# Optimization experiments

Measured on AMD Instinct MI355X. Metric: run time of the kernel, lower is better.

## Reference

```python
import jax, jax.numpy as jnp
import numpy as np

B, S, H, MAX_LEN = 32, 1024, 384, 8192


def setup_inputs() -> dict:
    key = jax.random.key(0)
    k0, k1, k2 = jax.random.split(key, 3)
    x = jax.random.normal(k0, (B, S, H), dtype=jnp.float32)
    src_mask = jnp.ones((B, S), dtype=bool)
    mel_mask = jnp.ones((B, MAX_LEN), dtype=bool)
    duration_target = jax.random.randint(k1, (B, S), 0, 8)
    pitch_target = jax.random.normal(k2, (B, MAX_LEN), dtype=jnp.float32)
    return {
        "x": x,
        "src_mask": src_mask,
        "mel_mask": mel_mask,
        "duration_target": duration_target,
        "pitch_target": pitch_target,
        "max_len": MAX_LEN,
    }


def _length_regulate(x, duration, max_len):
    """Vectorized repeat_interleave + pad.

    Frame t of batch b copies source vector j where
    cumsum(duration)[b, j-1] <= t < cumsum(duration)[b, j].
    """
    cum = jnp.cumsum(duration, axis=1)                      # [B, S]
    mel_len = cum[:, -1]                                    # [B]
    t = jnp.arange(max_len)                                 # [MAX]
    # searchsorted(side='right') maps frame index -> source index
    idx = jax.vmap(lambda c: jnp.searchsorted(c, t, side="right"))(cum)  # [B, MAX]
    idx = jnp.minimum(idx, x.shape[1] - 1)
    out = jnp.take_along_axis(x, idx[:, :, None], axis=1)   # [B, MAX, H]
    valid = t[None, :] < mel_len[:, None]                   # [B, MAX]  (zero padding)
    out = jnp.where(valid[:, :, None], out, jnp.zeros((), out.dtype))
    return out, mel_len


def reference(x, src_mask, mel_mask, duration_target, pitch_target, max_len):
    out, mel_len = _length_regulate(x, duration_target, max_len)
    return (out, mel_len, mel_mask)
```

## Files before the change

### kernel.cpp

```cpp
#include <hip/hip_runtime.h>

#define BB 32
#define SS 1024
#define HH 384
#define MAXLEN 8192
#define H4 (HH / 4)
#define OUT0 (BB * MAXLEN * HH)
#define MEL_OFF OUT0
#define MASK_OFF (OUT0 + BB)

typedef float vfloat4 __attribute__((ext_vector_type(4)));

__global__ __launch_bounds__(1024) void k_prep(
    const int* __restrict__ dur,
    const int* __restrict__ mel_mask_in,
    float* __restrict__ out,
    int* __restrict__ idxbuf)
{
    __shared__ int cum[SS];
    const int b = blockIdx.x;
    const int tid = threadIdx.x;

    cum[tid] = dur[b * SS + tid];
    for (int off = 1; off < SS; off <<= 1) {
        __syncthreads();
        int v = (tid >= off) ? cum[tid - off] : 0;
        __syncthreads();
        cum[tid] += v;
    }
    __syncthreads();

    const int mel_len = cum[SS - 1];
    if (tid == 0) out[MEL_OFF + b] = (float)mel_len;

    for (int k = 0; k < MAXLEN / SS; ++k) {
        const int t = tid + k * SS;
        int lo = 0, hi = SS;
        while (lo < hi) {
            int mid = (lo + hi) >> 1;
            if (cum[mid] <= t) lo = mid + 1; else hi = mid;
        }
        int idx = (lo < SS) ? lo : (SS - 1);
        idxbuf[b * MAXLEN + t] = (t < mel_len) ? idx : -1;
        out[MASK_OFF + b * MAXLEN + t] = mel_mask_in[b * MAXLEN + t] ? 1.0f : 0.0f;
    }
}

#define NB_EXP 24576
__global__ __launch_bounds__(256) void k_expand(
    const vfloat4* __restrict__ x4,
    const int* __restrict__ idxbuf,
    vfloat4* __restrict__ out4)
{
    const int L = blockIdx.x;
    const int W = (L & 7) * (NB_EXP / 8) + (L >> 3);
    const int base = W * 1024 + (int)threadIdx.x;
#pragma unroll
    for (int j = 0; j < 4; ++j) {
        const int i = base + j * 256;
        const int ft = i / H4;
        const int c  = i - ft * H4;
        const int id = idxbuf[ft];
        vfloat4 v = (vfloat4)(0.f);
        if (id >= 0) {
            const int b = ft >> 13;
            v = x4[(size_t)(b * SS + id) * H4 + c];
        }
        __builtin_nontemporal_store(v, &out4[i]);
    }
}

extern "C" void kernel_launch(void* const* d_in, const int* in_sizes, int n_in,
                              void* d_out, int out_size, void* d_ws, size_t ws_size,
                              hipStream_t stream) {
    const float* x = (const float*)d_in[0];
    const int* mel_mask_in = (const int*)d_in[2];
    const int* dur = (const int*)d_in[3];
    float* out = (float*)d_out;
    int* idxbuf = (int*)d_ws;

    k_prep<<<BB, 1024, 0, stream>>>(dur, mel_mask_in, out, idxbuf);
    k_expand<<<NB_EXP, 256, 0, stream>>>((const vfloat4*)x, idxbuf, (vfloat4*)out);
}
```

Baseline: 446.6 us.

## Fuse index computation and frame expansion into a single kernel

Merges the prefix-sum/searchsorted prep kernel with the expansion copy kernel. Each of 256 blocks recomputes its batch's cumulative durations, resolves indices for its 1024 frames into shared memory, then copies the frames. This removes the second launch and the global index buffer round trip, and spreads the prep across more blocks. In exchange the scan is computed redundantly eight times per batch, and the copy runs with only 256 large blocks, which may limit memory-level parallelism.

```diff
diff --git a/kernel.cpp b/kernel.cpp
--- a/kernel.cpp
+++ b/kernel.cpp
@@ -8,17 +8,23 @@
 #define OUT0 (BB * MAXLEN * HH)
 #define MEL_OFF OUT0
 #define MASK_OFF (OUT0 + BB)
+#define FRAMES_PER_BLK 1024
+#define NBLK (BB * (MAXLEN / FRAMES_PER_BLK))
 
 typedef float vfloat4 __attribute__((ext_vector_type(4)));
 
-__global__ __launch_bounds__(1024) void k_prep(
+__global__ __launch_bounds__(1024) void k_fused(
+    const vfloat4* __restrict__ x4,
     const int* __restrict__ dur,
     const int* __restrict__ mel_mask_in,
-    float* __restrict__ out,
-    int* __restrict__ idxbuf)
+    float* __restrict__ out)
 {
     __shared__ int cum[SS];
-    const int b = blockIdx.x;
+    __shared__ int idxl[FRAMES_PER_BLK];
+
+    const int blk = blockIdx.x;
+    const int b = blk >> 3;
+    const int s = blk & 7;
     const int tid = threadIdx.x;
 
     cum[tid] = dur[b * SS + tid];
@@ -31,42 +37,30 @@
     __syncthreads();
 
     const int mel_len = cum[SS - 1];
-    if (tid == 0) out[MEL_OFF + b] = (float)mel_len;
+    if (s == 0 && tid == 0) out[MEL_OFF + b] = (float)mel_len;
 
-    for (int k = 0; k < MAXLEN / SS; ++k) {
-        const int t = tid + k * SS;
-        int lo = 0, hi = SS;
-        while (lo < hi) {
-            int mid = (lo + hi) >> 1;
-            if (cum[mid] <= t) lo = mid + 1; else hi = mid;
-        }
-        int idx = (lo < SS) ? lo : (SS - 1);
-        idxbuf[b * MAXLEN + t] = (t < mel_len) ? idx : -1;
-        out[MASK_OFF + b * MAXLEN + t] = mel_mask_in[b * MAXLEN + t] ? 1.0f : 0.0f;
+    const int t = s * FRAMES_PER_BLK + tid;
+    out[MASK_OFF + b * MAXLEN + t] = mel_mask_in[b * MAXLEN + t] ? 1.0f : 0.0f;
+
+    int lo = 0, hi = SS;
+    while (lo < hi) {
+        int mid = (lo + hi) >> 1;
+        if (cum[mid] <= t) lo = mid + 1; else hi = mid;
     }
-}
+    int idx = (lo < SS) ? lo : (SS - 1);
+    idxl[tid] = (t < mel_len) ? idx : -1;
+    __syncthreads();
 
-#define NB_EXP 24576
-__global__ __launch_bounds__(256) void k_expand(
-    const vfloat4* __restrict__ x4,
-    const int* __restrict__ idxbuf,
-    vfloat4* __restrict__ out4)
-{
-    const int L = blockIdx.x;
-    const int W = (L & 7) * (NB_EXP / 8) + (L >> 3);
-    const int base = W * 1024 + (int)threadIdx.x;
-#pragma unroll
-    for (int j = 0; j < 4; ++j) {
-        const int i = base + j * 256;
-        const int ft = i / H4;
-        const int c  = i - ft * H4;
-        const int id = idxbuf[ft];
+    const size_t out_base = (size_t)(b * MAXLEN + s * FRAMES_PER_BLK) * H4;
+    const size_t x_base = (size_t)b * SS * H4;
+    vfloat4* __restrict__ out4 = (vfloat4*)out;
+    for (int j = tid; j < FRAMES_PER_BLK * H4; j += 1024) {
+        const int fl = j / H4;
+        const int c  = j - fl * H4;
+        const int id = idxl[fl];
         vfloat4 v = (vfloat4)(0.f);
-        if (id >= 0) {
-            const int b = ft >> 13;
-            v = x4[(size_t)(b * SS + id) * H4 + c];
-        }
-        __builtin_nontemporal_store(v, &out4[i]);
+        if (id >= 0) v = x4[x_base + (size_t)id * H4 + c];
+        __builtin_nontemporal_store(v, &out4[out_base + j]);
     }
 }
 
@@ -77,8 +71,6 @@
     const int* mel_mask_in = (const int*)d_in[2];
     const int* dur = (const int*)d_in[3];
     float* out = (float*)d_out;
-    int* idxbuf = (int*)d_ws;
 
-    k_prep<<<BB, 1024, 0, stream>>>(dur, mel_mask_in, out, idxbuf);
-    k_expand<<<NB_EXP, 256, 0, stream>>>((const vfloat4*)x, idxbuf, (vfloat4*)out);
+    k_fused<<<NBLK, 1024, 0, stream>>>((const vfloat4*)x, dur, mel_mask_in, out);
 }
```

After: 480.9 us. 7.7% more time.
